# Kernel optimization log

Hardware: AMD Instinct MI355X
Metric: run time of the kernel (lower is better)

The kernel has to match this reference:

```python
import jax, jax.numpy as jnp
import numpy as np

B, H, W, C = 8, 64, 64, 256
NUM_HEADS = 8
HEAD_DIM = C // NUM_HEADS
H_SP, W_SP = 64, 8  # idx=0: h_sp=H, w_sp=split_size[1]
SCALE = HEAD_DIM ** -0.5


def img2windows(img):
    # img: [B, C, H, W] -> [B*nW, h_sp*w_sp, C]
    b, c, h, w = img.shape
    x = img.reshape(b, c, h // H_SP, H_SP, w // W_SP, W_SP)
    x = jnp.transpose(x, (0, 2, 4, 3, 5, 1))
    return x.reshape(-1, H_SP * W_SP, c)


def im2cswin(x):
    # x: [B, L, C] -> [B*nW, heads, h_sp*w_sp, head_dim]
    xi = jnp.transpose(x, (0, 2, 1)).reshape(B, C, H, W)
    xw = img2windows(xi)
    xw = xw.reshape(-1, H_SP * W_SP, NUM_HEADS, HEAD_DIM)
    return jnp.transpose(xw, (0, 2, 1, 3))


def get_lepe(x, conv_w, conv_b):
    xi = jnp.transpose(x, (0, 2, 1)).reshape(B, C, H, W)
    xi = xi.reshape(B, C, H // H_SP, H_SP, W // W_SP, W_SP)
    xi = jnp.transpose(xi, (0, 2, 4, 1, 3, 5)).reshape(-1, C, H_SP, W_SP)
    # depthwise 3x3 conv, padding 1
    lepe = jax.lax.conv_general_dilated(
        xi, conv_w, window_strides=(1, 1), padding=((1, 1), (1, 1)),
        feature_group_count=C, dimension_numbers=('NCHW', 'OIHW', 'NCHW'))
    lepe = lepe + conv_b[None, :, None, None]
    def to_heads(t):
        t = t.reshape(-1, NUM_HEADS, HEAD_DIM, H_SP * W_SP)
        return jnp.transpose(t, (0, 1, 3, 2))
    return to_heads(xi), to_heads(lepe)


def windows2img(xw):
    # xw: [B*nW, h_sp*w_sp, C] -> [B, H, W, C]
    x = xw.reshape(B, H // H_SP, W // W_SP, H_SP, W_SP, C)
    x = jnp.transpose(x, (0, 1, 3, 2, 4, 5))
    return x.reshape(B, H, W, C)


def setup_inputs() -> dict:
    key = jax.random.key(0)
    k1, k2, k3 = jax.random.split(key, 3)
    x = jax.random.normal(k1, (3, B, H * W, C), dtype=jnp.float32)
    conv_w = jax.random.normal(k2, (C, 1, 3, 3), dtype=jnp.float32) * 0.1
    conv_b = jax.random.normal(k3, (C,), dtype=jnp.float32) * 0.1
    return {"x": x, "conv_w": conv_w, "conv_b": conv_b}


def reference(x, conv_w, conv_b):
    q, k, v = x[0], x[1], x[2]
    qh = im2cswin(q) * SCALE          # [nW*B, h, S, d]
    kh = im2cswin(k)
    vh, lepe = get_lepe(v, conv_w, conv_b)
    attn = jnp.einsum('whsd,whtd->whst', qh, kh)
    attn = jax.nn.softmax(attn, axis=-1)
    out = jnp.einsum('whst,whtd->whsd', attn, vh) + lepe
    out = jnp.transpose(out, (0, 2, 1, 3)).reshape(-1, H_SP * W_SP, C)
    return windows2img(out).reshape(B, H * W, C)
```

## Files before the change

kernel.cpp:

```cpp
#include <hip/hip_runtime.h>

typedef __attribute__((ext_vector_type(8))) __bf16 bf16x8;
typedef __attribute__((ext_vector_type(4))) __bf16 bf16x4;
typedef __attribute__((ext_vector_type(4))) float floatx4;

static __device__ __forceinline__ floatx4 mfma16(bf16x8 a, bf16x8 b, floatx4 c) {
    return __builtin_amdgcn_mfma_f32_16x16x32_bf16(a, b, c, 0, 0, 0);
}

#define QSCALE 0.25504099302278787f

__global__ __launch_bounds__(256, 2) void lepe_attn_kernel(
    const float* __restrict__ x, const float* __restrict__ conv_w,
    const float* __restrict__ conv_b, float* __restrict__ out)
{
    const int bx = blockIdx.x;
    const int wi = bx >> 3, hd = bx & 7;
    const int b = wi >> 3, wblk = wi & 7;
    const int tid = threadIdx.x;
    const int wave = tid >> 6, lane = tid & 63;
    const int g = lane >> 4, ln = lane & 15;

    __shared__ __align__(16) __bf16 Ks[512][32];
    __shared__ __align__(16) __bf16 VsT[32][520];
    __shared__ __align__(16) __bf16 Pc[4][32][36];
    __shared__ float Wc[32][9];
    __shared__ float Bc[32];

    const float* qp = x;
    const float* kp = x + 8 * 4096 * 256;
    const float* vp = x + 2 * 8 * 4096 * 256;
    const int base  = b * 4096 * 256;
    const int cbase = hd * 32;
    const int wcol0 = wblk * 8;

    for (int i = tid; i < 4096; i += 256) {
        int t = i >> 3, f = i & 7;
        int l = ((t >> 3) << 6) + wcol0 + (t & 7);
        int off = base + l * 256 + cbase + f * 4;
        float4 k4 = *(const float4*)(kp + off);
        bf16x4 kk = { (__bf16)k4.x, (__bf16)k4.y, (__bf16)k4.z, (__bf16)k4.w };
        *(bf16x4*)&Ks[t][f * 4] = kk;
        float4 v4 = *(const float4*)(vp + off);
        VsT[f*4+0][t] = (__bf16)v4.x;
        VsT[f*4+1][t] = (__bf16)v4.y;
        VsT[f*4+2][t] = (__bf16)v4.z;
        VsT[f*4+3][t] = (__bf16)v4.w;
    }
    for (int i = tid; i < 288; i += 256)
        Wc[i / 9][i % 9] = conv_w[(cbase + i / 9) * 9 + (i % 9)];
    if (tid < 32) Bc[tid] = conv_b[cbase + tid];
    __syncthreads();

    for (int qt = wave; qt < 16; qt += 4) {
        const int sbase = qt * 32;

        bf16x8 aq0, aq1;
        {
            int s = sbase + ln;
            int l = ((s >> 3) << 6) + wcol0 + (s & 7);
            const float* qb = qp + base + l * 256 + cbase + g * 8;
            float4 a = *(const float4*)qb, c = *(const float4*)(qb + 4);
            aq0[0] = (__bf16)(a.x * QSCALE); aq0[1] = (__bf16)(a.y * QSCALE);
            aq0[2] = (__bf16)(a.z * QSCALE); aq0[3] = (__bf16)(a.w * QSCALE);
            aq0[4] = (__bf16)(c.x * QSCALE); aq0[5] = (__bf16)(c.y * QSCALE);
            aq0[6] = (__bf16)(c.z * QSCALE); aq0[7] = (__bf16)(c.w * QSCALE);
            s = sbase + 16 + ln;
            l = ((s >> 3) << 6) + wcol0 + (s & 7);
            qb = qp + base + l * 256 + cbase + g * 8;
            a = *(const float4*)qb; c = *(const float4*)(qb + 4);
            aq1[0] = (__bf16)(a.x * QSCALE); aq1[1] = (__bf16)(a.y * QSCALE);
            aq1[2] = (__bf16)(a.z * QSCALE); aq1[3] = (__bf16)(a.w * QSCALE);
            aq1[4] = (__bf16)(c.x * QSCALE); aq1[5] = (__bf16)(c.y * QSCALE);
            aq1[6] = (__bf16)(c.z * QSCALE); aq1[7] = (__bf16)(c.w * QSCALE);
        }

        floatx4 o00 = {0.f,0.f,0.f,0.f}, o01 = {0.f,0.f,0.f,0.f};
        floatx4 o10 = {0.f,0.f,0.f,0.f}, o11 = {0.f,0.f,0.f,0.f};
        float ls0[4] = {0.f,0.f,0.f,0.f}, ls1[4] = {0.f,0.f,0.f,0.f};

        for (int kt = 0; kt < 8; kt++) {
            const floatx4 zf = {0.f,0.f,0.f,0.f};
            floatx4 sc0[4], sc1[4];
            #pragma unroll
            for (int f = 0; f < 4; f++) {
                bf16x8 bk = *(const bf16x8*)&Ks[kt * 64 + f * 16 + ln][g * 8];
                sc0[f] = mfma16(aq0, bk, zf);
                sc1[f] = mfma16(aq1, bk, zf);
            }
            #pragma unroll
            for (int c2 = 0; c2 < 2; c2++) {
                #pragma unroll
                for (int f2 = 0; f2 < 2; f2++) {
                    #pragma unroll
                    for (int r = 0; r < 4; r++) {
                        float p0 = __builtin_amdgcn_exp2f(sc0[c2 * 2 + f2][r]);
                        ls0[r] += p0;
                        Pc[wave][g * 4 + r][f2 * 16 + ln] = (__bf16)p0;
                        float p1 = __builtin_amdgcn_exp2f(sc1[c2 * 2 + f2][r]);
                        ls1[r] += p1;
                        Pc[wave][16 + g * 4 + r][f2 * 16 + ln] = (__bf16)p1;
                    }
                }
                __builtin_amdgcn_wave_barrier();
                bf16x4 al = *(const bf16x4*)&Pc[wave][ln][g * 8];
                bf16x4 ah = *(const bf16x4*)&Pc[wave][ln][g * 8 + 4];
                bf16x8 ap0 = {al[0],al[1],al[2],al[3],ah[0],ah[1],ah[2],ah[3]};
                al = *(const bf16x4*)&Pc[wave][16 + ln][g * 8];
                ah = *(const bf16x4*)&Pc[wave][16 + ln][g * 8 + 4];
                bf16x8 ap1 = {al[0],al[1],al[2],al[3],ah[0],ah[1],ah[2],ah[3]};
                bf16x8 bv0 = *(const bf16x8*)&VsT[ln][kt * 64 + c2 * 32 + g * 8];
                bf16x8 bv1 = *(const bf16x8*)&VsT[16 + ln][kt * 64 + c2 * 32 + g * 8];
                o00 = mfma16(ap0, bv0, o00);
                o01 = mfma16(ap0, bv1, o01);
                o10 = mfma16(ap1, bv0, o10);
                o11 = mfma16(ap1, bv1, o11);
                __builtin_amdgcn_wave_barrier();
            }
        }

        #pragma unroll
        for (int rs = 0; rs < 2; rs++) {
            floatx4 oa = rs ? o10 : o00;
            floatx4 ob = rs ? o11 : o01;
            const float* lsp = rs ? ls1 : ls0;
            #pragma unroll
            for (int r = 0; r < 4; r++) {
                float t = lsp[r];
                t += __shfl_xor(t, 1); t += __shfl_xor(t, 2);
                t += __shfl_xor(t, 4); t += __shfl_xor(t, 8);
                float inv = 1.0f / t;
                int s = sbase + rs * 16 + g * 4 + r;
                int h = s >> 3, w = s & 7;
                int l = h * 64 + wcol0 + w;
                #pragma unroll
                for (int half = 0; half < 2; half++) {
                    int dd = half * 16 + ln;
                    float lep = Bc[dd];
                    #pragma unroll
                    for (int ky = 0; ky < 3; ky++) {
                        int hh = h + ky - 1;
                        #pragma unroll
                        for (int kx = 0; kx < 3; kx++) {
                            int ww = w + kx - 1;
                            bool ok = (hh >= 0) & (hh < 64) & (ww >= 0) & (ww < 8);
                            float vv = ok ? (float)VsT[dd][hh * 8 + ww] : 0.f;
                            lep = fmaf(vv, Wc[dd][ky * 3 + kx], lep);
                        }
                    }
                    float oval = (half ? ob[r] : oa[r]) * inv + lep;
                    out[base + l * 256 + cbase + dd] = oval;
                }
            }
        }
    }
}

extern "C" void kernel_launch(void* const* d_in, const int* in_sizes, int n_in,
                              void* d_out, int out_size, void* d_ws, size_t ws_size,
                              hipStream_t stream) {
    const float* x  = (const float*)d_in[0];
    const float* cw = (const float*)d_in[1];
    const float* cb = (const float*)d_in[2];
    float* out = (float*)d_out;
    lepe_attn_kernel<<<dim3(512), dim3(256), 0, stream>>>(x, cw, cb, out);
}
```

Before: 197.3 us.

## Compute transposed scores so P feeds PV MFMA from registers, dropping LDS staging

```diff
diff --git a/kernel.cpp b/kernel.cpp
--- a/kernel.cpp
+++ b/kernel.cpp
@@ -2,10 +2,14 @@
 
 typedef __attribute__((ext_vector_type(8))) __bf16 bf16x8;
 typedef __attribute__((ext_vector_type(4))) __bf16 bf16x4;
+typedef __attribute__((ext_vector_type(4))) _Float16 half4;
 typedef __attribute__((ext_vector_type(4))) float floatx4;
 
-static __device__ __forceinline__ floatx4 mfma16(bf16x8 a, bf16x8 b, floatx4 c) {
+static __device__ __forceinline__ floatx4 mfma_qk(bf16x8 a, bf16x8 b, floatx4 c) {
     return __builtin_amdgcn_mfma_f32_16x16x32_bf16(a, b, c, 0, 0, 0);
+}
+static __device__ __forceinline__ floatx4 mfma_pv(half4 a, half4 b, floatx4 c) {
+    return __builtin_amdgcn_mfma_f32_16x16x16f16(a, b, c, 0, 0, 0);
 }
 
 #define QSCALE 0.25504099302278787f
@@ -21,9 +25,8 @@
     const int wave = tid >> 6, lane = tid & 63;
     const int g = lane >> 4, ln = lane & 15;
 
-    __shared__ __align__(16) __bf16 Ks[512][32];
-    __shared__ __align__(16) __bf16 VsT[32][520];
-    __shared__ __align__(16) __bf16 Pc[4][32][36];
+    __shared__ __align__(16) __bf16   Ks[512][32];
+    __shared__ __align__(16) _Float16 VsT[32][522];
     __shared__ float Wc[32][9];
     __shared__ float Bc[32];
 
@@ -42,116 +45,110 @@
         bf16x4 kk = { (__bf16)k4.x, (__bf16)k4.y, (__bf16)k4.z, (__bf16)k4.w };
         *(bf16x4*)&Ks[t][f * 4] = kk;
         float4 v4 = *(const float4*)(vp + off);
-        VsT[f*4+0][t] = (__bf16)v4.x;
-        VsT[f*4+1][t] = (__bf16)v4.y;
-        VsT[f*4+2][t] = (__bf16)v4.z;
-        VsT[f*4+3][t] = (__bf16)v4.w;
+        VsT[f*4+0][t] = (_Float16)v4.x;
+        VsT[f*4+1][t] = (_Float16)v4.y;
+        VsT[f*4+2][t] = (_Float16)v4.z;
+        VsT[f*4+3][t] = (_Float16)v4.w;
     }
     for (int i = tid; i < 288; i += 256)
         Wc[i / 9][i % 9] = conv_w[(cbase + i / 9) * 9 + (i % 9)];
     if (tid < 32) Bc[tid] = conv_b[cbase + tid];
     __syncthreads();
 
-    for (int qt = wave; qt < 16; qt += 4) {
-        const int sbase = qt * 32;
-
-        bf16x8 aq0, aq1;
+    for (int qc = wave; qc < 16; qc += 4) {
+        bf16x8 bq0, bq1;
         {
-            int s = sbase + ln;
+            int s = qc * 32 + ln;
             int l = ((s >> 3) << 6) + wcol0 + (s & 7);
             const float* qb = qp + base + l * 256 + cbase + g * 8;
             float4 a = *(const float4*)qb, c = *(const float4*)(qb + 4);
-            aq0[0] = (__bf16)(a.x * QSCALE); aq0[1] = (__bf16)(a.y * QSCALE);
-            aq0[2] = (__bf16)(a.z * QSCALE); aq0[3] = (__bf16)(a.w * QSCALE);
-            aq0[4] = (__bf16)(c.x * QSCALE); aq0[5] = (__bf16)(c.y * QSCALE);
-            aq0[6] = (__bf16)(c.z * QSCALE); aq0[7] = (__bf16)(c.w * QSCALE);
-            s = sbase + 16 + ln;
+            bq0[0] = (__bf16)(a.x * QSCALE); bq0[1] = (__bf16)(a.y * QSCALE);
+            bq0[2] = (__bf16)(a.z * QSCALE); bq0[3] = (__bf16)(a.w * QSCALE);
+            bq0[4] = (__bf16)(c.x * QSCALE); bq0[5] = (__bf16)(c.y * QSCALE);
+            bq0[6] = (__bf16)(c.z * QSCALE); bq0[7] = (__bf16)(c.w * QSCALE);
+            s = qc * 32 + 16 + ln;
             l = ((s >> 3) << 6) + wcol0 + (s & 7);
             qb = qp + base + l * 256 + cbase + g * 8;
             a = *(const float4*)qb; c = *(const float4*)(qb + 4);
-            aq1[0] = (__bf16)(a.x * QSCALE); aq1[1] = (__bf16)(a.y * QSCALE);
-            aq1[2] = (__bf16)(a.z * QSCALE); aq1[3] = (__bf16)(a.w * QSCALE);
-            aq1[4] = (__bf16)(c.x * QSCALE); aq1[5] = (__bf16)(c.y * QSCALE);
-            aq1[6] = (__bf16)(c.z * QSCALE); aq1[7] = (__bf16)(c.w * QSCALE);
+            bq1[0] = (__bf16)(a.x * QSCALE); bq1[1] = (__bf16)(a.y * QSCALE);
+            bq1[2] = (__bf16)(a.z * QSCALE); bq1[3] = (__bf16)(a.w * QSCALE);
+            bq1[4] = (__bf16)(c.x * QSCALE); bq1[5] = (__bf16)(c.y * QSCALE);
+            bq1[6] = (__bf16)(c.z * QSCALE); bq1[7] = (__bf16)(c.w * QSCALE);
         }
 
-        floatx4 o00 = {0.f,0.f,0.f,0.f}, o01 = {0.f,0.f,0.f,0.f};
-        floatx4 o10 = {0.f,0.f,0.f,0.f}, o11 = {0.f,0.f,0.f,0.f};
-        float ls0[4] = {0.f,0.f,0.f,0.f}, ls1[4] = {0.f,0.f,0.f,0.f};
+        floatx4 aLo0 = {0.f,0.f,0.f,0.f}, aHi0 = {0.f,0.f,0.f,0.f};
+        floatx4 aLo1 = {0.f,0.f,0.f,0.f}, aHi1 = {0.f,0.f,0.f,0.f};
+        float lsum0 = 0.f, lsum1 = 0.f;
+        const floatx4 zf = {0.f,0.f,0.f,0.f};
 
-        for (int kt = 0; kt < 8; kt++) {
-            const floatx4 zf = {0.f,0.f,0.f,0.f};
-            floatx4 sc0[4], sc1[4];
+        #pragma unroll 4
+        for (int tb = 0; tb < 32; tb++) {
+            bf16x8 ak = *(const bf16x8*)&Ks[tb * 16 + ln][g * 8];
+            floatx4 sc0 = mfma_qk(ak, bq0, zf);
+            floatx4 sc1 = mfma_qk(ak, bq1, zf);
+
+            half4 ph0, ph1;
             #pragma unroll
-            for (int f = 0; f < 4; f++) {
-                bf16x8 bk = *(const bf16x8*)&Ks[kt * 64 + f * 16 + ln][g * 8];
-                sc0[f] = mfma16(aq0, bk, zf);
-                sc1[f] = mfma16(aq1, bk, zf);
+            for (int r = 0; r < 4; r++) {
+                float p0 = __builtin_amdgcn_exp2f(sc0[r]);
+                lsum0 += p0; ph0[r] = (_Float16)p0;
+                float p1 = __builtin_amdgcn_exp2f(sc1[r]);
+                lsum1 += p1; ph1[r] = (_Float16)p1;
             }
+
+            int tcol = tb * 16 + g * 4;
+            const unsigned* r0 = (const unsigned*)&VsT[ln][0];
+            const unsigned* r1 = (const unsigned*)&VsT[16 + ln][0];
+            half4 av0, av1;
+            ((unsigned*)&av0)[0] = r0[tcol >> 1];
+            ((unsigned*)&av0)[1] = r0[(tcol >> 1) + 1];
+            ((unsigned*)&av1)[0] = r1[tcol >> 1];
+            ((unsigned*)&av1)[1] = r1[(tcol >> 1) + 1];
+
+            aLo0 = mfma_pv(av0, ph0, aLo0);
+            aHi0 = mfma_pv(av1, ph0, aHi0);
+            aLo1 = mfma_pv(av0, ph1, aLo1);
+            aHi1 = mfma_pv(av1, ph1, aHi1);
+        }
+
+        lsum0 += __shfl_xor(lsum0, 16); lsum0 += __shfl_xor(lsum0, 32);
+        lsum1 += __shfl_xor(lsum1, 16); lsum1 += __shfl_xor(lsum1, 32);
+        float inv0 = 1.0f / lsum0, inv1 = 1.0f / lsum1;
+
+        #pragma unroll
+        for (int ss = 0; ss < 2; ss++) {
+            int s = qc * 32 + ss * 16 + ln;
+            int h = s >> 3, w = s & 7;
+            int l = h * 64 + wcol0 + w;
+            float inv = ss ? inv1 : inv0;
+            floatx4 alo = ss ? aLo1 : aLo0;
+            floatx4 ahi = ss ? aHi1 : aHi0;
+            float4 olo, ohi;
             #pragma unroll
-            for (int c2 = 0; c2 < 2; c2++) {
+            for (int r = 0; r < 4; r++) {
+                int ddl = g * 4 + r;
+                float lepl = Bc[ddl];
+                float leph = Bc[16 + ddl];
                 #pragma unroll
-                for (int f2 = 0; f2 < 2; f2++) {
+                for (int ky = 0; ky < 3; ky++) {
+                    int hh = h + ky - 1;
+                    bool okh = (hh >= 0) & (hh < 64);
                     #pragma unroll
-                    for (int r = 0; r < 4; r++) {
-                        float p0 = __builtin_amdgcn_exp2f(sc0[c2 * 2 + f2][r]);
-                        ls0[r] += p0;
-                        Pc[wave][g * 4 + r][f2 * 16 + ln] = (__bf16)p0;
-                        float p1 = __builtin_amdgcn_exp2f(sc1[c2 * 2 + f2][r]);
-                        ls1[r] += p1;
-                        Pc[wave][16 + g * 4 + r][f2 * 16 + ln] = (__bf16)p1;
+                    for (int kx = 0; kx < 3; kx++) {
+                        int ww = w + kx - 1;
+                        bool ok = okh & (ww >= 0) & (ww < 8);
+                        float vl = ok ? (float)VsT[ddl][hh * 8 + ww] : 0.f;
+                        float vh = ok ? (float)VsT[16 + ddl][hh * 8 + ww] : 0.f;
+                        lepl = fmaf(vl, Wc[ddl][ky * 3 + kx], lepl);
+                        leph = fmaf(vh, Wc[16 + ddl][ky * 3 + kx], leph);
                     }
                 }
-                __builtin_amdgcn_wave_barrier();
-                bf16x4 al = *(const bf16x4*)&Pc[wave][ln][g * 8];
-                bf16x4 ah = *(const bf16x4*)&Pc[wave][ln][g * 8 + 4];
-                bf16x8 ap0 = {al[0],al[1],al[2],al[3],ah[0],ah[1],ah[2],ah[3]};
-                al = *(const bf16x4*)&Pc[wave][16 + ln][g * 8];
-                ah = *(const bf16x4*)&Pc[wave][16 + ln][g * 8 + 4];
-                bf16x8 ap1 = {al[0],al[1],al[2],al[3],ah[0],ah[1],ah[2],ah[3]};
-                bf16x8 bv0 = *(const bf16x8*)&VsT[ln][kt * 64 + c2 * 32 + g * 8];
-                bf16x8 bv1 = *(const bf16x8*)&VsT[16 + ln][kt * 64 + c2 * 32 + g * 8];
-                o00 = mfma16(ap0, bv0, o00);
-                o01 = mfma16(ap0, bv1, o01);
-                o10 = mfma16(ap1, bv0, o10);
-                o11 = mfma16(ap1, bv1, o11);
-                __builtin_amdgcn_wave_barrier();
+                ((float*)&olo)[r] = alo[r] * inv + lepl;
+                ((float*)&ohi)[r] = ahi[r] * inv + leph;
             }
-        }
-
-        #pragma unroll
-        for (int rs = 0; rs < 2; rs++) {
-            floatx4 oa = rs ? o10 : o00;
-            floatx4 ob = rs ? o11 : o01;
-            const float* lsp = rs ? ls1 : ls0;
-            #pragma unroll
-            for (int r = 0; r < 4; r++) {
-                float t = lsp[r];
-                t += __shfl_xor(t, 1); t += __shfl_xor(t, 2);
-                t += __shfl_xor(t, 4); t += __shfl_xor(t, 8);
-                float inv = 1.0f / t;
-                int s = sbase + rs * 16 + g * 4 + r;
-                int h = s >> 3, w = s & 7;
-                int l = h * 64 + wcol0 + w;
-                #pragma unroll
-                for (int half = 0; half < 2; half++) {
-                    int dd = half * 16 + ln;
-                    float lep = Bc[dd];
-                    #pragma unroll
-                    for (int ky = 0; ky < 3; ky++) {
-                        int hh = h + ky - 1;
-                        #pragma unroll
-                        for (int kx = 0; kx < 3; kx++) {
-                            int ww = w + kx - 1;
-                            bool ok = (hh >= 0) & (hh < 64) & (ww >= 0) & (ww < 8);
-                            float vv = ok ? (float)VsT[dd][hh * 8 + ww] : 0.f;
-                            lep = fmaf(vv, Wc[dd][ky * 3 + kx], lep);
-                        }
-                    }
-                    float oval = (half ? ob[r] : oa[r]) * inv + lep;
-                    out[base + l * 256 + cbase + dd] = oval;
-                }
-            }
+            float* ob = out + base + l * 256 + cbase;
+            *(float4*)(ob + g * 4) = olo;
+            *(float4*)(ob + 16 + g * 4) = ohi;
         }
     }
 }
```

Result: faster. 185.2 us (-6.1%).
